# Kernel optimization log

Hardware: AMD Instinct MI355X
Metric: run time of the kernel (lower is better)

## Reference

```python
import jax, jax.numpy as jnp
import numpy as np

B, S, HID = 4, 1024, 2048
H, KV, D = 16, 4, 128  # query heads, kv heads, head_dim
ROPE_THETA = 1e6


def setup_inputs() -> dict:
    key = jax.random.key(0)
    ks = jax.random.split(key, 5)
    x = jax.random.normal(ks[0], (B, S, HID), dtype=jnp.float32)
    wq = jax.random.normal(ks[1], (HID, H * D), dtype=jnp.float32) / np.sqrt(HID)
    wk = jax.random.normal(ks[2], (HID, KV * D), dtype=jnp.float32) / np.sqrt(HID)
    wv = jax.random.normal(ks[3], (HID, KV * D), dtype=jnp.float32) / np.sqrt(HID)
    wo = jax.random.normal(ks[4], (H * D, HID), dtype=jnp.float32) / np.sqrt(H * D)
    # RoPE tables: freqs duplicated to head_dim (HF convention matching rotate_half)
    inv_freq = 1.0 / (ROPE_THETA ** (jnp.arange(0, D, 2, dtype=jnp.float32) / D))
    ang = jnp.arange(S, dtype=jnp.float32)[:, None] * inv_freq[None, :]  # [S, D/2]
    emb = jnp.concatenate([ang, ang], axis=-1)  # [S, D]
    return {"x": x, "cos": jnp.cos(emb), "sin": jnp.sin(emb),
            "wq": wq, "wk": wk, "wv": wv, "wo": wo}


def _rotate_half(t):
    half = t.shape[-1] // 2
    return jnp.concatenate([-t[..., half:], t[..., :half]], axis=-1)


def reference(x, cos, sin, wq, wk, wv, wo):
    b, s, _ = x.shape
    q = (x @ wq).reshape(b, s, H, D)
    k = (x @ wk).reshape(b, s, KV, D)
    v = (x @ wv).reshape(b, s, KV, D)
    # RoPE: cos/sin [S,D] broadcast over heads (unsqueeze_dim=1 -> [S,1,D])
    c = cos[:, None, :]
    sn = sin[:, None, :]
    q = q * c + _rotate_half(q) * sn
    k = k * c + _rotate_half(k) * sn
    # repeat_kv: each kv head repeated n_repeat times consecutively
    rep = H // KV
    k = jnp.repeat(k, rep, axis=2)  # [B,S,H,D]
    v = jnp.repeat(v, rep, axis=2)
    # [B,H,S,D]
    q = q.transpose(0, 2, 1, 3)
    k = k.transpose(0, 2, 1, 3)
    v = v.transpose(0, 2, 1, 3)
    scores = jnp.einsum("bhqd,bhkd->bhqk", q, k) / jnp.sqrt(jnp.float32(D))
    causal = jnp.tril(jnp.ones((s, s), dtype=bool))
    scores = jnp.where(causal, scores, -jnp.inf)
    probs = jax.nn.softmax(scores.astype(jnp.float32), axis=-1).astype(q.dtype)
    out = jnp.einsum("bhqk,bhkd->bhqd", probs, v)
    out = out.transpose(0, 2, 1, 3).reshape(b, s, H * D)
    return out @ wo
```

## Files before the change

kernel.cpp:

```cpp
#include <hip/hip_runtime.h>

typedef __attribute__((ext_vector_type(8))) __bf16 bf16x8;
typedef __attribute__((ext_vector_type(4))) __bf16 bf16x4;
typedef __attribute__((ext_vector_type(4))) float f32x4;

#define DEV static __device__ __forceinline__

DEV void gload_lds16(const void* g, void* l) {
  __builtin_amdgcn_global_load_lds((const __attribute__((address_space(1))) void*)g,
                                   (__attribute__((address_space(3))) void*)l, 16, 0, 0);
}

DEV void lgkm0_sb() {
  asm volatile("s_waitcnt lgkmcnt(0)" ::: "memory");
  __builtin_amdgcn_sched_barrier(0);
}

__global__ void cvt_kernel(const float* __restrict__ src, __bf16* __restrict__ dst, int n) {
  int i = (blockIdx.x * 256 + threadIdx.x) * 8;
  if (i >= n) return;
  float4 a = *(const float4*)(src + i);
  float4 b = *(const float4*)(src + i + 4);
  bf16x8 o;
  o[0] = (__bf16)a.x; o[1] = (__bf16)a.y; o[2] = (__bf16)a.z; o[3] = (__bf16)a.w;
  o[4] = (__bf16)b.x; o[5] = (__bf16)b.y; o[6] = (__bf16)b.z; o[7] = (__bf16)b.w;
  *(bf16x8*)(dst + i) = o;
}

__global__ void tcvt_kernel(const float* __restrict__ src, __bf16* __restrict__ dst, int K, int N) {
  __shared__ float tile[32][33];
  int k0 = blockIdx.y * 32, n0 = blockIdx.x * 32;
  int tx = threadIdx.x & 31, ty = threadIdx.x >> 5;
  #pragma unroll
  for (int i = 0; i < 32; i += 8)
    tile[ty + i][tx] = src[(size_t)(k0 + ty + i) * N + n0 + tx];
  __syncthreads();
  #pragma unroll
  for (int i = 0; i < 32; i += 8)
    dst[(size_t)(n0 + ty + i) * K + k0 + tx] = (__bf16)tile[tx][ty + i];
}

__global__ void vt_kernel(const __bf16* __restrict__ QKV, __bf16* __restrict__ VT) {
  __shared__ __bf16 t[32][33];
  int sx = blockIdx.x;
  int dx = blockIdx.y;
  int bk = blockIdx.z;
  int b = bk >> 2, kvh = bk & 3;
  int tx = threadIdx.x & 31, ty = threadIdx.x >> 5;
  #pragma unroll
  for (int i = 0; i < 32; i += 8)
    t[ty + i][tx] = QKV[(size_t)(b * 1024 + sx * 32 + ty + i) * 3072 + 2560 + kvh * 128 + dx * 32 + tx];
  __syncthreads();
  #pragma unroll
  for (int i = 0; i < 32; i += 8)
    VT[((size_t)bk * 128 + dx * 32 + ty + i) * 1024 + sx * 32 + tx] = t[tx][ty + i];
}

__global__ __launch_bounds__(512, 2) void gemm8p_qkv(const __bf16* __restrict__ A,
                                                     const __bf16* __restrict__ Bt,
                                                     __bf16* __restrict__ C,
                                                     int M, int N, int K) {
  constexpr int ABYTES = 256 * 64 * 2;
  constexpr int BBYTES = 192 * 64 * 2;
  __shared__ alignas(1024) char smem[2 * (ABYTES + BBYTES)];

  const int tid = threadIdx.x;
  const int l = tid & 63, w = tid >> 6;
  const int wr = w >> 2, wc = w & 3;
  const int g = l >> 4, ln = l & 15;

  const int nbx = gridDim.x;
  const int nwg = nbx * gridDim.y;
  int lin = blockIdx.y * nbx + blockIdx.x;
  lin = (lin & 7) * (nwg >> 3) + (lin >> 3);
  const int brow = (lin / nbx) * 256, bcol = (lin % nbx) * 192;

  const __bf16* Ag = A + (size_t)brow * K;
  const __bf16* Bg = Bt + (size_t)bcol * K;
  const int NT = K / 64;

  f32x4 acc[8][3] = {};

  auto chunk = [&](const __bf16* gb, char* lb, int ktc, int sub) {
    int r16 = l >> 2;
    int colb = ((l & 3) * 16) ^ (((l >> 5) & 1) << 5);
    int row = (sub >> 1) * 16 + r16;
    gload_lds16(gb + (size_t)row * K + ktc * 64 + (sub & 1) * 32 + (colb >> 1),
                lb + sub * 1024 + l * 16);
  };
  auto stA0 = [&](int ktc, char* ab) {
    #pragma unroll
    for (int i = 0; i < 2; ++i) { int idx = i * 8 + w; chunk(Ag, ab, ktc, (idx >> 3) * 16 + (idx & 7)); }
  };
  auto stA1 = [&](int ktc, char* ab) {
    #pragma unroll
    for (int i = 0; i < 2; ++i) { int idx = i * 8 + w; chunk(Ag, ab, ktc, 8 + (idx >> 3) * 16 + (idx & 7)); }
  };
  auto stBg0 = [&](int ktc, char* bb) {
    #pragma unroll
    for (int i = 0; i < 2; ++i) {
      int t = i * 8 + w;
      int sub = ((t >> 2) * 3 + ((t >> 1) & 1)) * 2 + (t & 1);
      chunk(Bg, bb, ktc, sub);
    }
  };
  auto stBg1 = [&](int ktc, char* bb) {
    int sub = ((w >> 1) * 3 + 2) * 2 + (w & 1);
    chunk(Bg, bb, ktc, sub);
  };

  auto ldA = [&](const char* ab, int m, int kk) -> bf16x8 {
    int sub = (wr * 8 + m) * 2 + kk;
    return *(const bf16x8*)(ab + sub * 1024 + ln * 64 + ((g * 16) ^ (((ln >> 3) & 1) << 5)));
  };
  auto ldB = [&](const char* bb, int nf, int kk) -> bf16x8 {
    int sub = (wc * 3 + nf) * 2 + kk;
    return *(const bf16x8*)(bb + sub * 1024 + ln * 64 + ((g * 16) ^ (((ln >> 3) & 1) << 5)));
  };

  auto bar = [&]() {
    __builtin_amdgcn_sched_barrier(0);
    __builtin_amdgcn_s_barrier();
    __builtin_amdgcn_sched_barrier(0);
  };

  char* const A0 = smem;
  char* const A1 = smem + ABYTES;
  char* const B0 = smem + 2 * ABYTES;
  char* const B1 = smem + 2 * ABYTES + BBYTES;

  stA0(0, A0); stBg0(0, B0); stBg1(0, B0); stA1(0, A0);
  stA0(1, A1); stBg0(1, B1); stBg1(1, B1); stA1(1, A1);
  asm volatile("s_waitcnt vmcnt(10)" ::: "memory");
  __builtin_amdgcn_sched_barrier(0);
  bar();

  bf16x8 af[4][2], bfv[3][2];

#define QKV_TILE(KT, AB, BB)                                                                      \
  do {                                                                                            \
    const int ktc = ((KT) + 2) & 31;                                                              \
                                               \
    _Pragma("unroll")                                                                             \
    for (int m = 0; m < 4; ++m) { af[m][0] = ldA(AB, m, 0); af[m][1] = ldA(AB, m, 1); }           \
    _Pragma("unroll")                                                                             \
    for (int nf = 0; nf < 2; ++nf) { bfv[nf][0] = ldB(BB, nf, 0); bfv[nf][1] = ldB(BB, nf, 1); }  \
    bar();                                                                                        \
    lgkm0_sb();                                                                                   \
    __builtin_amdgcn_s_setprio(1);                                                                \
    _Pragma("unroll")                                                                             \
    for (int m = 0; m < 4; ++m)                                                                   \
      _Pragma("unroll")                                                                           \
      for (int nf = 0; nf < 2; ++nf)                                                              \
        _Pragma("unroll")                                                                         \
        for (int kk = 0; kk < 2; ++kk)                                                            \
          acc[m][nf] = __builtin_amdgcn_mfma_f32_16x16x32_bf16(af[m][kk], bfv[nf][kk],            \
                                                               acc[m][nf], 0, 0, 0);              \
    __builtin_amdgcn_s_setprio(0);                                                                \
    asm volatile("s_waitcnt vmcnt(9)" ::: "memory");                                              \
    __builtin_amdgcn_sched_barrier(0);                                                            \
    bar();                                                                                        \
                                        \
    bfv[2][0] = ldB(BB, 2, 0); bfv[2][1] = ldB(BB, 2, 1);                                         \
    stA0(ktc, AB); stBg0(ktc, BB);                                                                \
    bar();                                                                                        \
    lgkm0_sb();                                                                                   \
    __builtin_amdgcn_s_setprio(1);                                                                \
    _Pragma("unroll")                                                                             \
    for (int m = 0; m < 4; ++m)                                                                   \
      _Pragma("unroll")                                                                           \
      for (int kk = 0; kk < 2; ++kk)                                                              \
        acc[m][2] = __builtin_amdgcn_mfma_f32_16x16x32_bf16(af[m][kk], bfv[2][kk],                \
                                                            acc[m][2], 0, 0, 0);                  \
    __builtin_amdgcn_s_setprio(0);                                                                \
    asm volatile("s_waitcnt vmcnt(11)" ::: "memory");                                             \
    __builtin_amdgcn_sched_barrier(0);                                                            \
    bar();                                                                                        \
                                                \
    _Pragma("unroll")                                                                             \
    for (int m = 0; m < 4; ++m) { af[m][0] = ldA(AB, 4 + m, 0); af[m][1] = ldA(AB, 4 + m, 1); }   \
    stBg1(ktc, BB);                                                                               \
    bar();                                                                                        \
    lgkm0_sb();                                                                                   \
    __builtin_amdgcn_s_setprio(1);                                                                \
    _Pragma("unroll")                                                                             \
    for (int m = 0; m < 4; ++m)                                                                   \
      _Pragma("unroll")                                                                           \
      for (int nf = 0; nf < 2; ++nf)                                                              \
        _Pragma("unroll")                                                                         \
        for (int kk = 0; kk < 2; ++kk)                                                            \
          acc[4 + m][nf] = __builtin_amdgcn_mfma_f32_16x16x32_bf16(af[m][kk], bfv[nf][kk],        \
                                                                   acc[4 + m][nf], 0, 0, 0);      \
    __builtin_amdgcn_s_setprio(0);                                                                \
    bar();                                                                                        \
                                              \
    stA1(ktc, AB);                                                                                \
    bar();                                                                                        \
    lgkm0_sb();                                                                                   \
    __builtin_amdgcn_s_setprio(1);                                                                \
    _Pragma("unroll")                                                                             \
    for (int m = 0; m < 4; ++m)                                                                   \
      _Pragma("unroll")                                                                           \
      for (int kk = 0; kk < 2; ++kk)                                                              \
        acc[4 + m][2] = __builtin_amdgcn_mfma_f32_16x16x32_bf16(af[m][kk], bfv[2][kk],            \
                                                                acc[4 + m][2], 0, 0, 0);          \
    __builtin_amdgcn_s_setprio(0);                                                                \
    asm volatile("s_waitcnt vmcnt(10)" ::: "memory");                                             \
    __builtin_amdgcn_sched_barrier(0);                                                            \
    bar();                                                                                        \
  } while (0)

  for (int ktp = 0; ktp < NT; ktp += 2) {
    QKV_TILE(ktp, A0, B0);
    QKV_TILE(ktp + 1, A1, B1);
  }
#undef QKV_TILE

  #pragma unroll
  for (int mi = 0; mi < 8; ++mi)
    #pragma unroll
    for (int nf = 0; nf < 3; ++nf)
      #pragma unroll
      for (int j = 0; j < 4; ++j) {
        size_t r = brow + wr * 128 + mi * 16 + g * 4 + j;
        size_t c = bcol + wc * 48 + nf * 16 + ln;
        C[r * N + c] = (__bf16)acc[mi][nf][j];
      }
}

__global__ __launch_bounds__(512, 2) void gemm2p(const __bf16* __restrict__ A,
                                                 const __bf16* __restrict__ Bt,
                                                 float* __restrict__ C,
                                                 int M, int N, int K) {
  constexpr int ABYTES = 256 * 64 * 2;
  constexpr int BBYTES = 128 * 64 * 2;
  __shared__ alignas(1024) char smem[2 * (ABYTES + BBYTES)];

  const int tid = threadIdx.x;
  const int l = tid & 63, w = tid >> 6;
  const int wr = w >> 1, wc = w & 1;
  const int g = l >> 4, ln = l & 15;

  const int nbx = gridDim.x;
  const int nwg = nbx * gridDim.y;
  int lin = blockIdx.y * nbx + blockIdx.x;
  lin = (lin & 7) * (nwg >> 3) + (lin >> 3);
  const int brow = (lin / nbx) * 256, bcol = (lin % nbx) * 128;

  const __bf16* Ag = A + (size_t)brow * K;
  const __bf16* Bg = Bt + (size_t)bcol * K;
  const int NT = K / 64;

  f32x4 acc[4][4] = {};

  auto chunk = [&](const __bf16* gb, char* lb, int ktc, int sub) {
    int r16 = l >> 2;
    int colb = ((l & 3) * 16) ^ (((l >> 5) & 1) << 5);
    int row = (sub >> 1) * 16 + r16;
    gload_lds16(gb + (size_t)row * K + ktc * 64 + (sub & 1) * 32 + (colb >> 1),
                lb + sub * 1024 + l * 16);
  };
  auto stAp0 = [&](int ktc, char* ab) {
    #pragma unroll
    for (int i = 0; i < 2; ++i) { int t = i * 8 + w; chunk(Ag, ab, ktc, (t >> 2) * 8 + (t & 3)); }
  };
  auto stAp1 = [&](int ktc, char* ab) {
    #pragma unroll
    for (int i = 0; i < 2; ++i) { int t = i * 8 + w; chunk(Ag, ab, ktc, (t >> 2) * 8 + 4 + (t & 3)); }
  };
  auto stB = [&](int ktc, char* bb) {
    #pragma unroll
    for (int i = 0; i < 2; ++i) { int t = i * 8 + w; chunk(Bg, bb, ktc, t); }
  };

  auto ldA = [&](const char* ab, int mi, int kk) -> bf16x8 {
    int sub = (wr * 4 + mi) * 2 + kk;
    return *(const bf16x8*)(ab + sub * 1024 + ln * 64 + ((g * 16) ^ (((ln >> 3) & 1) << 5)));
  };
  auto ldB = [&](const char* bb, int nf, int kk) -> bf16x8 {
    int sub = (wc * 4 + nf) * 2 + kk;
    return *(const bf16x8*)(bb + sub * 1024 + ln * 64 + ((g * 16) ^ (((ln >> 3) & 1) << 5)));
  };

  auto vm6 = [&]() {
    asm volatile("s_waitcnt vmcnt(6)" ::: "memory");
    __builtin_amdgcn_sched_barrier(0);
  };
  auto bar = [&]() {
    __builtin_amdgcn_sched_barrier(0);
    __builtin_amdgcn_s_barrier();
    __builtin_amdgcn_sched_barrier(0);
  };

  char* const A0 = smem;
  char* const A1 = smem + ABYTES;
  char* const B0 = smem + 2 * ABYTES;
  char* const B1 = smem + 2 * ABYTES + BBYTES;

  stAp0(0, A0); stB(0, B0);
  stAp1(0, A0);
  stAp0(1, A1); stB(1, B1);
  vm6();
  bar();

  bf16x8 af[2][2], bfv[4][2];

#define OP_TILE(KT, AB, BB, ABo)                                                                  \
  do {                                                                                            \
    const int ktc1 = ((KT) + 1) & 31;                                                             \
    const int ktc2 = ((KT) + 2) & 31;                                                             \
                                   \
    _Pragma("unroll")                                                                             \
    for (int mi = 0; mi < 2; ++mi) { af[mi][0] = ldA(AB, mi, 0); af[mi][1] = ldA(AB, mi, 1); }    \
    _Pragma("unroll")                                                                             \
    for (int nf = 0; nf < 4; ++nf) { bfv[nf][0] = ldB(BB, nf, 0); bfv[nf][1] = ldB(BB, nf, 1); }  \
    stAp1(ktc1, ABo);                                                                             \
    bar();                                                                                        \
    lgkm0_sb();                                                                                   \
    __builtin_amdgcn_s_setprio(1);                                                                \
    _Pragma("unroll")                                                                             \
    for (int mi = 0; mi < 2; ++mi)                                                                \
      _Pragma("unroll")                                                                           \
      for (int nf = 0; nf < 4; ++nf)                                                              \
        _Pragma("unroll")                                                                         \
        for (int kk = 0; kk < 2; ++kk)                                                            \
          acc[mi][nf] = __builtin_amdgcn_mfma_f32_16x16x32_bf16(af[mi][kk], bfv[nf][kk],          \
                                                                acc[mi][nf], 0, 0, 0);            \
    __builtin_amdgcn_s_setprio(0);                                                                \
    vm6();                                                                                        \
    bar();                                                                                        \
                                    \
    _Pragma("unroll")                                                                             \
    for (int mi = 0; mi < 2; ++mi) { af[mi][0] = ldA(AB, 2 + mi, 0); af[mi][1] = ldA(AB, 2 + mi, 1); } \
    stAp0(ktc2, AB); stB(ktc2, BB);                                                               \
    bar();                                                                                        \
    lgkm0_sb();                                                                                   \
    __builtin_amdgcn_s_setprio(1);                                                                \
    _Pragma("unroll")                                                                             \
    for (int mi = 0; mi < 2; ++mi)                                                                \
      _Pragma("unroll")                                                                           \
      for (int nf = 0; nf < 4; ++nf)                                                              \
        _Pragma("unroll")                                                                         \
        for (int kk = 0; kk < 2; ++kk)                                                            \
          acc[2 + mi][nf] = __builtin_amdgcn_mfma_f32_16x16x32_bf16(af[mi][kk], bfv[nf][kk],      \
                                                                    acc[2 + mi][nf], 0, 0, 0);    \
    __builtin_amdgcn_s_setprio(0);                                                                \
    vm6();                                                                                        \
    bar();                                                                                        \
  } while (0)

  for (int ktp = 0; ktp < NT; ktp += 2) {
    OP_TILE(ktp, A0, B0, A1);
    OP_TILE(ktp + 1, A1, B1, A0);
  }
#undef OP_TILE

  #pragma unroll
  for (int mi = 0; mi < 4; ++mi)
    #pragma unroll
    for (int nf = 0; nf < 4; ++nf)
      #pragma unroll
      for (int j = 0; j < 4; ++j) {
        size_t r = brow + wr * 64 + mi * 16 + g * 4 + j;
        size_t c = bcol + wc * 64 + nf * 16 + ln;
        C[r * N + c] = acc[mi][nf][j];
      }
}

__global__ void ropek_kernel(__bf16* __restrict__ QKV, const float* __restrict__ cosb,
                             const float* __restrict__ sinb) {
  int gid = blockIdx.x * 256 + threadIdx.x;
  int p = gid & 15;
  int ht = gid >> 4;
  int hc = ht & 3;
  int tok = ht >> 2;
  int s = tok & 1023;
  __bf16* base = QKV + (size_t)tok * 3072 + 2048 + hc * 128;
  int d0 = p * 4;
  const float* cr = cosb + s * 128;
  const float* sr = sinb + s * 128;
  float x0[4], x1[4];
  #pragma unroll
  for (int j = 0; j < 4; ++j) {
    x0[j] = (float)base[d0 + j];
    x1[j] = (float)base[d0 + 64 + j];
  }
  #pragma unroll
  for (int j = 0; j < 4; ++j) {
    float n0 = x0[j] * cr[d0 + j] - x1[j] * sr[d0 + j];
    float n1 = x1[j] * cr[d0 + 64 + j] + x0[j] * sr[d0 + 64 + j];
    base[d0 + j] = (__bf16)n0;
    base[d0 + 64 + j] = (__bf16)n1;
  }
}

__global__ __launch_bounds__(256, 2) void attn_kernel(const __bf16* __restrict__ QKV,
                                                      const __bf16* __restrict__ VT,
                                                      const float* __restrict__ cosb,
                                                      const float* __restrict__ sinb,
                                                      __bf16* __restrict__ AO) {
  __shared__ __bf16 Kl[2][64 * 128];
  __shared__ __bf16 Vt[128 * 64];
  __shared__ __bf16 Pl[4][16 * 72];

  const int tid = threadIdx.x, l = tid & 63, w = tid >> 6;
  const int h = blockIdx.y, b = blockIdx.z;
  const int kvh = h >> 2;
  const int g = l >> 4, ln = l & 15;
  const __bf16* VTg = VT + (size_t)(b * 4 + kvh) * 128 * 1024;
  const float scsc = 0.08838834764831845f;

  auto stageK = [&](int buf, int kt) {
    const __bf16* Kg = QKV + (size_t)(b * 1024 + kt * 64) * 3072 + 2048 + kvh * 128;
    #pragma unroll
    for (int i = 0; i < 4; ++i) {
      int r = i * 16 + (tid >> 4);
      int c = tid & 15;
      int csw = c ^ (r & 7);
      gload_lds16(Kg + (size_t)r * 3072 + csw * 8, (char*)&Kl[buf][0] + i * 4096 + tid * 16);
    }
  };
  auto stageV = [&](int kt) {
    #pragma unroll
    for (int i = 0; i < 4; ++i) {
      int ci = i * 256 + tid;
      int row = ci >> 3;
      int c = ci & 7;
      int csw = c ^ (row & 7);
      gload_lds16(VTg + (size_t)row * 1024 + kt * 64 + csw * 8, (char*)Vt + (size_t)ci * 16);
    }
  };

  #pragma unroll 1
  for (int pass = 0; pass < 2; ++pass) {
    const int qt = pass ? 15 - (int)blockIdx.x : (int)blockIdx.x;
    const size_t tokQ = (size_t)b * 1024 + qt * 64;
    const int srow = qt * 64 + w * 16 + ln;

    bf16x8 qf[4];
    {
      const __bf16* qp = QKV + (tokQ + w * 16 + ln) * 3072 + h * 128;
      bf16x8 qraw[4];
      #pragma unroll
      for (int ks = 0; ks < 4; ++ks) qraw[ks] = *(const bf16x8*)(qp + ks * 32 + g * 8);
      const float* cr = cosb + (size_t)srow * 128;
      const float* sr = sinb + (size_t)srow * 128;
      #pragma unroll
      for (int ks2 = 0; ks2 < 2; ++ks2)
        #pragma unroll
        for (int j = 0; j < 8; ++j) {
          int d = ks2 * 32 + g * 8 + j;
          float lo = (float)qraw[ks2][j], hi = (float)qraw[ks2 + 2][j];
          float c0 = cr[d], s0 = sr[d];
          qf[ks2][j]     = (__bf16)(lo * c0 - hi * s0);
          qf[ks2 + 2][j] = (__bf16)(hi * c0 + lo * s0);
        }
    }

    float mrow = -1e30f, lrow = 0.f;
    f32x4 acco[8] = {};

    stageK(0, 0);
    int cur = 0;

    for (int kt = 0; kt <= qt; ++kt) {
      __syncthreads();

      stageV(kt);
      if (kt < qt) stageK(cur ^ 1, kt + 1);

      f32x4 accs[4] = {};
      __builtin_amdgcn_s_setprio(1);
      #pragma unroll
      for (int cb = 0; cb < 4; ++cb) {
        int row = cb * 16 + ln;
        #pragma unroll
        for (int ks = 0; ks < 4; ++ks) {
          bf16x8 kb = *(const bf16x8*)((const char*)&Kl[cur][0] + row * 256 +
                                       (((ks * 4 + g) ^ (row & 7)) * 16));
          accs[cb] = __builtin_amdgcn_mfma_f32_16x16x32_bf16(kb, qf[ks], accs[cb], 0, 0, 0);
        }
      }
      __builtin_amdgcn_s_setprio(0);

      const bool diag = (kt == qt);
      #pragma unroll
      for (int cb = 0; cb < 4; ++cb)
        #pragma unroll
        for (int j = 0; j < 4; ++j) {
          float s = accs[cb][j] * scsc;
          if (diag && (cb * 16 + g * 4 + j > w * 16 + ln)) s = -1e30f;
          accs[cb][j] = s;
        }

      float mt = accs[0][0];
      #pragma unroll
      for (int cb = 0; cb < 4; ++cb)
        #pragma unroll
        for (int j = 0; j < 4; ++j) mt = fmaxf(mt, accs[cb][j]);
      mt = fmaxf(mt, __shfl_xor(mt, 16, 64));
      mt = fmaxf(mt, __shfl_xor(mt, 32, 64));
      float mnew = fmaxf(mrow, mt);
      float corr = __expf(mrow - mnew);
      mrow = mnew;
      float rs = 0.f;
      #pragma unroll
      for (int cb = 0; cb < 4; ++cb)
        #pragma unroll
        for (int j = 0; j < 4; ++j) {
          float p = __expf(accs[cb][j] - mnew);
          accs[cb][j] = p;
          rs += p;
        }
      rs += __shfl_xor(rs, 16, 64);
      rs += __shfl_xor(rs, 32, 64);
      lrow = lrow * corr + rs;
      #pragma unroll
      for (int n = 0; n < 8; ++n)
        #pragma unroll
        for (int j = 0; j < 4; ++j) acco[n][j] *= corr;

      #pragma unroll
      for (int cb = 0; cb < 4; ++cb) {
        bf16x4 pw;
        #pragma unroll
        for (int j = 0; j < 4; ++j) pw[j] = (__bf16)accs[cb][j];
        *(bf16x4*)(&Pl[w][ln * 72 + cb * 16 + g * 4]) = pw;
      }

      __syncthreads();

      __builtin_amdgcn_s_setprio(1);
      #pragma unroll
      for (int sc = 0; sc < 2; ++sc) {
        bf16x8 pa = *(const bf16x8*)(&Pl[w][ln * 72 + sc * 32 + g * 8]);
        #pragma unroll
        for (int n = 0; n < 8; ++n) {
          int row = n * 16 + ln;
          bf16x8 vb = *(const bf16x8*)((const char*)Vt + row * 128 +
                                       (((sc * 4 + g) ^ (row & 7)) * 16));
          acco[n] = __builtin_amdgcn_mfma_f32_16x16x32_bf16(vb, pa, acco[n], 0, 0, 0);
        }
      }
      __builtin_amdgcn_s_setprio(0);
      cur ^= 1;
    }

    float rl = 1.f / lrow;
    size_t r = tokQ + w * 16 + ln;
    #pragma unroll
    for (int n = 0; n < 8; ++n) {
      bf16x4 ov;
      #pragma unroll
      for (int j = 0; j < 4; ++j) ov[j] = (__bf16)(acco[n][j] * rl);
      *(bf16x4*)(&AO[r * 2048 + h * 128 + n * 16 + g * 4]) = ov;
    }
  }
}

extern "C" void kernel_launch(void* const* d_in, const int* in_sizes, int n_in,
                              void* d_out, int out_size, void* d_ws, size_t ws_size,
                              hipStream_t stream) {
  const float* x    = (const float*)d_in[0];
  const float* cosb = (const float*)d_in[1];
  const float* sinb = (const float*)d_in[2];
  const float* wq   = (const float*)d_in[3];
  const float* wk   = (const float*)d_in[4];
  const float* wv   = (const float*)d_in[5];
  const float* wo   = (const float*)d_in[6];
  float* out = (float*)d_out;

  char* ws = (char*)d_ws;
  const size_t OFF_XB    = 0;
  const size_t OFF_WQKVT = OFF_XB + 16777216;
  const size_t OFF_WOT   = OFF_WQKVT + 12582912;
  const size_t OFF_QKV   = OFF_WOT + 8388608;
  const size_t OFF_AO    = OFF_QKV + 25165824;
  const size_t OFF_VT    = OFF_XB;

  __bf16* Xb    = (__bf16*)(ws + OFF_XB);
  __bf16* WqkvT = (__bf16*)(ws + OFF_WQKVT);
  __bf16* WoT   = (__bf16*)(ws + OFF_WOT);
  __bf16* QKVb  = (__bf16*)(ws + OFF_QKV);
  __bf16* AOb   = (__bf16*)(ws + OFF_AO);
  __bf16* VTb   = (__bf16*)(ws + OFF_VT);

  cvt_kernel<<<4096 * 2048 / 8 / 256, 256, 0, stream>>>(x, Xb, 4096 * 2048);
  tcvt_kernel<<<dim3(64, 64), 256, 0, stream>>>(wq, WqkvT, 2048, 2048);
  tcvt_kernel<<<dim3(16, 64), 256, 0, stream>>>(wk, WqkvT + (size_t)2048 * 2048, 2048, 512);
  tcvt_kernel<<<dim3(16, 64), 256, 0, stream>>>(wv, WqkvT + (size_t)2560 * 2048, 2048, 512);
  tcvt_kernel<<<dim3(64, 64), 256, 0, stream>>>(wo, WoT, 2048, 2048);
  gemm8p_qkv<<<dim3(16, 16), 512, 0, stream>>>(Xb, WqkvT, QKVb, 4096, 3072, 2048);
  vt_kernel<<<dim3(32, 4, 16), 256, 0, stream>>>(QKVb, VTb);
  ropek_kernel<<<4096 * 4 * 16 / 256, 256, 0, stream>>>(QKVb, cosb, sinb);
  attn_kernel<<<dim3(8, 16, 4), 256, 0, stream>>>(QKVb, VTb, cosb, sinb, AOb);
  gemm2p<<<dim3(16, 16), 512, 0, stream>>>(AOb, WoT, out, 4096, 2048, 2048);
}
```

Measured before the change: 168.9 us.

## Fuse weight transposes, double-buffer V tiles, and skip softmax rescales

Merges the four weight transpose-convert launches into one grid to cut launch overhead. In attention, V tiles are now double-buffered and prefetched alongside K, so V loads overlap the previous tile's compute. The block-wide barrier before the PV MMA is replaced with a per-wave LDS wait. A lazy-rescale rule skips the running max and accumulator correction unless the new max exceeds the old by more than 8. This uses more LDS and relies on the per-wave P buffer being private; the lazy rescale lets exponent values grow up to e^8 before renormalising.

```diff
diff --git a/kernel.cpp b/kernel.cpp
--- a/kernel.cpp
+++ b/kernel.cpp
@@ -27,9 +27,19 @@
   *(bf16x8*)(dst + i) = o;
 }
 
-__global__ void tcvt_kernel(const float* __restrict__ src, __bf16* __restrict__ dst, int K, int N) {
+__global__ void tcvt_all(const float* __restrict__ wq, const float* __restrict__ wk,
+                         const float* __restrict__ wv, const float* __restrict__ wo,
+                         __bf16* __restrict__ WqkvT, __bf16* __restrict__ WoT) {
   __shared__ float tile[32][33];
-  int k0 = blockIdx.y * 32, n0 = blockIdx.x * 32;
+  int bx = blockIdx.x;
+  const float* src;
+  __bf16* dst;
+  int N, n0, drow;
+  if (bx < 64)      { src = wq; dst = WqkvT; N = 2048; n0 = bx * 32;        drow = n0; }
+  else if (bx < 80) { src = wk; dst = WqkvT; N = 512;  n0 = (bx - 64) * 32; drow = 2048 + n0; }
+  else if (bx < 96) { src = wv; dst = WqkvT; N = 512;  n0 = (bx - 80) * 32; drow = 2560 + n0; }
+  else              { src = wo; dst = WoT;   N = 2048; n0 = (bx - 96) * 32; drow = n0; }
+  int k0 = blockIdx.y * 32;
   int tx = threadIdx.x & 31, ty = threadIdx.x >> 5;
   #pragma unroll
   for (int i = 0; i < 32; i += 8)
@@ -37,7 +47,7 @@
   __syncthreads();
   #pragma unroll
   for (int i = 0; i < 32; i += 8)
-    dst[(size_t)(n0 + ty + i) * K + k0 + tx] = (__bf16)tile[tx][ty + i];
+    dst[(size_t)(drow + ty + i) * 2048 + k0 + tx] = (__bf16)tile[tx][ty + i];
 }
 
 __global__ void vt_kernel(const __bf16* __restrict__ QKV, __bf16* __restrict__ VT) {
@@ -140,7 +150,6 @@
 #define QKV_TILE(KT, AB, BB)                                                                      \
   do {                                                                                            \
     const int ktc = ((KT) + 2) & 31;                                                              \
-                                               \
     _Pragma("unroll")                                                                             \
     for (int m = 0; m < 4; ++m) { af[m][0] = ldA(AB, m, 0); af[m][1] = ldA(AB, m, 1); }           \
     _Pragma("unroll")                                                                             \
@@ -160,7 +169,6 @@
     asm volatile("s_waitcnt vmcnt(9)" ::: "memory");                                              \
     __builtin_amdgcn_sched_barrier(0);                                                            \
     bar();                                                                                        \
-                                        \
     bfv[2][0] = ldB(BB, 2, 0); bfv[2][1] = ldB(BB, 2, 1);                                         \
     stA0(ktc, AB); stBg0(ktc, BB);                                                                \
     bar();                                                                                        \
@@ -176,7 +184,6 @@
     asm volatile("s_waitcnt vmcnt(11)" ::: "memory");                                             \
     __builtin_amdgcn_sched_barrier(0);                                                            \
     bar();                                                                                        \
-                                                \
     _Pragma("unroll")                                                                             \
     for (int m = 0; m < 4; ++m) { af[m][0] = ldA(AB, 4 + m, 0); af[m][1] = ldA(AB, 4 + m, 1); }   \
     stBg1(ktc, BB);                                                                               \
@@ -193,7 +200,6 @@
                                                                    acc[4 + m][nf], 0, 0, 0);      \
     __builtin_amdgcn_s_setprio(0);                                                                \
     bar();                                                                                        \
-                                              \
     stA1(ktc, AB);                                                                                \
     bar();                                                                                        \
     lgkm0_sb();                                                                                   \
@@ -309,7 +315,6 @@
   do {                                                                                            \
     const int ktc1 = ((KT) + 1) & 31;                                                             \
     const int ktc2 = ((KT) + 2) & 31;                                                             \
-                                   \
     _Pragma("unroll")                                                                             \
     for (int mi = 0; mi < 2; ++mi) { af[mi][0] = ldA(AB, mi, 0); af[mi][1] = ldA(AB, mi, 1); }    \
     _Pragma("unroll")                                                                             \
@@ -329,7 +334,6 @@
     __builtin_amdgcn_s_setprio(0);                                                                \
     vm6();                                                                                        \
     bar();                                                                                        \
-                                    \
     _Pragma("unroll")                                                                             \
     for (int mi = 0; mi < 2; ++mi) { af[mi][0] = ldA(AB, 2 + mi, 0); af[mi][1] = ldA(AB, 2 + mi, 1); } \
     stAp0(ktc2, AB); stB(ktc2, BB);                                                               \
@@ -400,7 +404,7 @@
                                                       const float* __restrict__ sinb,
                                                       __bf16* __restrict__ AO) {
   __shared__ __bf16 Kl[2][64 * 128];
-  __shared__ __bf16 Vt[128 * 64];
+  __shared__ __bf16 Vt[2][128 * 64];
   __shared__ __bf16 Pl[4][16 * 72];
 
   const int tid = threadIdx.x, l = tid & 63, w = tid >> 6;
@@ -420,14 +424,14 @@
       gload_lds16(Kg + (size_t)r * 3072 + csw * 8, (char*)&Kl[buf][0] + i * 4096 + tid * 16);
     }
   };
-  auto stageV = [&](int kt) {
+  auto stageV = [&](int buf, int kt) {
     #pragma unroll
     for (int i = 0; i < 4; ++i) {
       int ci = i * 256 + tid;
       int row = ci >> 3;
       int c = ci & 7;
       int csw = c ^ (row & 7);
-      gload_lds16(VTg + (size_t)row * 1024 + kt * 64 + csw * 8, (char*)Vt + (size_t)ci * 16);
+      gload_lds16(VTg + (size_t)row * 1024 + kt * 64 + csw * 8, (char*)&Vt[buf][0] + (size_t)ci * 16);
     }
   };
 
@@ -460,14 +464,14 @@
     float mrow = -1e30f, lrow = 0.f;
     f32x4 acco[8] = {};
 
-    stageK(0, 0);
+    __syncthreads();
+    stageK(0, 0); stageV(0, 0);
     int cur = 0;
 
     for (int kt = 0; kt <= qt; ++kt) {
       __syncthreads();
 
-      stageV(kt);
-      if (kt < qt) stageK(cur ^ 1, kt + 1);
+      if (kt < qt) { stageK(cur ^ 1, kt + 1); stageV(cur ^ 1, kt + 1); }
 
       f32x4 accs[4] = {};
       __builtin_amdgcn_s_setprio(1);
@@ -500,25 +504,28 @@
         for (int j = 0; j < 4; ++j) mt = fmaxf(mt, accs[cb][j]);
       mt = fmaxf(mt, __shfl_xor(mt, 16, 64));
       mt = fmaxf(mt, __shfl_xor(mt, 32, 64));
-      float mnew = fmaxf(mrow, mt);
-      float corr = __expf(mrow - mnew);
-      mrow = mnew;
+      if (!__all(mt <= mrow + 8.0f)) {
+        float mnew = fmaxf(mrow, mt);
+        float corr = __expf(mrow - mnew);
+        mrow = mnew;
+        lrow *= corr;
+        #pragma unroll
+        for (int n = 0; n < 8; ++n)
+          #pragma unroll
+          for (int j = 0; j < 4; ++j) acco[n][j] *= corr;
+      }
       float rs = 0.f;
       #pragma unroll
       for (int cb = 0; cb < 4; ++cb)
         #pragma unroll
         for (int j = 0; j < 4; ++j) {
-          float p = __expf(accs[cb][j] - mnew);
+          float p = __expf(accs[cb][j] - mrow);
           accs[cb][j] = p;
           rs += p;
         }
       rs += __shfl_xor(rs, 16, 64);
       rs += __shfl_xor(rs, 32, 64);
-      lrow = lrow * corr + rs;
-      #pragma unroll
-      for (int n = 0; n < 8; ++n)
-        #pragma unroll
-        for (int j = 0; j < 4; ++j) acco[n][j] *= corr;
+      lrow += rs;
 
       #pragma unroll
       for (int cb = 0; cb < 4; ++cb) {
@@ -527,8 +534,7 @@
         for (int j = 0; j < 4; ++j) pw[j] = (__bf16)accs[cb][j];
         *(bf16x4*)(&Pl[w][ln * 72 + cb * 16 + g * 4]) = pw;
       }
-
-      __syncthreads();
+      lgkm0_sb();
 
       __builtin_amdgcn_s_setprio(1);
       #pragma unroll
@@ -537,7 +543,7 @@
         #pragma unroll
         for (int n = 0; n < 8; ++n) {
           int row = n * 16 + ln;
-          bf16x8 vb = *(const bf16x8*)((const char*)Vt + row * 128 +
+          bf16x8 vb = *(const bf16x8*)((const char*)&Vt[cur][0] + row * 128 +
                                        (((sc * 4 + g) ^ (row & 7)) * 16));
           acco[n] = __builtin_amdgcn_mfma_f32_16x16x32_bf16(vb, pa, acco[n], 0, 0, 0);
         }
@@ -586,10 +592,7 @@
   __bf16* VTb   = (__bf16*)(ws + OFF_VT);
 
   cvt_kernel<<<4096 * 2048 / 8 / 256, 256, 0, stream>>>(x, Xb, 4096 * 2048);
-  tcvt_kernel<<<dim3(64, 64), 256, 0, stream>>>(wq, WqkvT, 2048, 2048);
-  tcvt_kernel<<<dim3(16, 64), 256, 0, stream>>>(wk, WqkvT + (size_t)2048 * 2048, 2048, 512);
-  tcvt_kernel<<<dim3(16, 64), 256, 0, stream>>>(wv, WqkvT + (size_t)2560 * 2048, 2048, 512);
-  tcvt_kernel<<<dim3(64, 64), 256, 0, stream>>>(wo, WoT, 2048, 2048);
+  tcvt_all<<<dim3(160, 64), 256, 0, stream>>>(wq, wk, wv, wo, WqkvT, WoT);
   gemm8p_qkv<<<dim3(16, 16), 512, 0, stream>>>(Xb, WqkvT, QKVb, 4096, 3072, 2048);
   vt_kernel<<<dim3(32, 4, 16), 256, 0, stream>>>(QKVb, VTb);
   ropek_kernel<<<4096 * 4 * 16 / 256, 256, 0, stream>>>(QKVb, cosb, sinb);
```

Result: no change. 166.3 us (-1.6%).
